# Kernel optimization log

Measured on AMD Instinct MI355X. Metric: run time of the kernel, lower is better.

The kernel has to match this reference:

```python
import jax, jax.numpy as jnp
import numpy as np

H = 16          # num_heads
D = 64          # head_dim = dim // num_heads
ROPE_THETA = 10000.0
NEG = -1e9


def _rope_angles(n, d):
    # matches get_1d_rotary_pos_embed(head_dim, N): freqs_cis = polar(1, t outer (theta^-(2i/d)))
    inv_freq = 1.0 / (ROPE_THETA ** (jnp.arange(0, d, 2, dtype=jnp.float32) / d))  # [d/2]
    ang = jnp.arange(n, dtype=jnp.float32)[:, None] * inv_freq[None, :]            # [n, d/2]
    return jnp.cos(ang), jnp.sin(ang)


def _apply_rope(x, cos, sin):
    # x: [B,H,N,D]; complex rotation on adjacent pairs (use_real=False semantics)
    x0 = x[..., 0::2]
    x1 = x[..., 1::2]
    # broadcast cos/sin [N, D/2] over batch and heads
    r0 = x0 * cos - x1 * sin
    r1 = x0 * sin + x1 * cos
    return jnp.stack([r0, r1], axis=-1).reshape(x.shape)


def setup_inputs() -> dict:
    key = jax.random.key(0)
    ks = jax.random.split(key, 5)
    B, N, C = 4, 2048, 1024
    s_in = 1.0 / np.sqrt(C)
    return {
        "x": jax.random.normal(ks[0], (B, N, C), dtype=jnp.float32),
        "Wqkv_w": jax.random.normal(ks[1], (3 * C, C), dtype=jnp.float32) * s_in,
        "Wqkv_b": jax.random.normal(ks[2], (3 * C,), dtype=jnp.float32) * 0.01,
        "out_w": jax.random.normal(ks[3], (C, C), dtype=jnp.float32) * s_in,
        "out_b": jax.random.normal(ks[4], (C,), dtype=jnp.float32) * 0.01,
    }


def reference(x, Wqkv_w, Wqkv_b, out_w, out_b):
    B, N, C = x.shape
    scale = D ** -0.5
    # fused QKV projection: [B,N,3C] -> [3,B,H,N,D]
    qkv = (jnp.einsum('bnc,oc->bno', x, Wqkv_w) + Wqkv_b)
    qkv = qkv.reshape(B, N, 3, H, D).transpose(2, 0, 3, 1, 4)
    q, k, v = qkv[0], qkv[1], qkv[2]
    # qk_norm=False -> Identity
    cos, sin = _rope_angles(N, D)
    q = _apply_rope(q, cos, sin)
    k = _apply_rope(k, cos, sin)
    attn = jnp.einsum('bhqd,bhkd->bhqk', q * scale, k)      # [B,H,N,N]
    causal = jnp.triu(jnp.ones((N, N), dtype=bool), k=1)
    attn = jnp.where(causal[None, None], NEG, attn)
    attn = jax.nn.softmax(attn, axis=-1)
    o = jnp.einsum('bhqk,bhkd->bhqd', attn, v)              # [B,H,N,D]
    o = o.transpose(0, 2, 1, 3).reshape(B, N, C)
    return jnp.einsum('bnc,oc->bno', o, out_w) + out_b
```

## Files before the change

kernel.cpp:

```cpp
#include <hip/hip_runtime.h>
#include <hip/hip_bf16.h>

#define DEVI __device__ __forceinline__

typedef __attribute__((ext_vector_type(8))) short short8v;
typedef __attribute__((ext_vector_type(4))) float f32x4;
typedef __attribute__((ext_vector_type(2))) unsigned u32x2;

DEVI short f2bf(float f) {
  __hip_bfloat16 h = __float2bfloat16(f);
  return __builtin_bit_cast(short, h);
}
DEVI float bf2f(short s) {
  unsigned u = ((unsigned)(unsigned short)s) << 16;
  return __builtin_bit_cast(float, u);
}
DEVI unsigned packbf(float a, float b) {
  return (unsigned)(unsigned short)f2bf(a) | ((unsigned)(unsigned short)f2bf(b) << 16);
}
DEVI void gload16(const void* g, void* l) {
  __builtin_amdgcn_global_load_lds((const __attribute__((address_space(1))) void*)g,
                                   (__attribute__((address_space(3))) void*)l, 16, 0, 0);
}
#define MFMA16(a, b, c) __builtin_amdgcn_mfma_f32_16x16x32_bf16((a), (b), (c), 0, 0, 0)


__global__ void cvt_all(const float* __restrict__ x, const float* __restrict__ wq,
                        const float* __restrict__ wo, short* __restrict__ xb,
                        short* __restrict__ wqb, short* __restrict__ wob) {
  int i = blockIdx.x * blockDim.x + threadIdx.x;
  const float* in;
  short* out;
  if (i < 2097152) { in = x; out = xb; }
  else if (i < 2097152 + 786432) { in = wq; out = wqb; i -= 2097152; }
  else { in = wo; out = wob; i -= 2097152 + 786432; }
  float4 v = ((const float4*)in)[i];
  short4 o;
  o.x = f2bf(v.x); o.y = f2bf(v.y); o.z = f2bf(v.z); o.w = f2bf(v.w);
  ((short4*)out)[i] = o;
}

__global__ void rope_table(float2* __restrict__ tbl) {
  int i = blockIdx.x * blockDim.x + threadIdx.x;
  int n = i >> 5, f = i & 31;
  float inv = powf(10000.0f, -(float)f * (1.0f / 32.0f));
  float ang = (float)n * inv;
  tbl[i] = make_float2(cosf(ang), sinf(ang));
}

__global__ void rope_k(short* __restrict__ kk, const float2* __restrict__ tbl) {
  int i = blockIdx.x * blockDim.x + threadIdx.x;
  int row = i >> 3, c8 = i & 7;
  int n = row & 2047;
  short* ad = kk + (size_t)row * 64 + c8 * 8;
  short8v vv = *(short8v*)ad;
  short8v ov;
#pragma unroll
  for (int j = 0; j < 4; ++j) {
    float2 cs = tbl[n * 32 + c8 * 4 + j];
    float x0 = bf2f(vv[2 * j]), x1 = bf2f(vv[2 * j + 1]);
    ov[2 * j]     = f2bf(x0 * cs.x - x1 * cs.y);
    ov[2 * j + 1] = f2bf(x0 * cs.y + x1 * cs.x);
  }
  *(short8v*)ad = ov;
}

__global__ __launch_bounds__(512, 2)
void gemm256(const short* __restrict__ A, const short* __restrict__ Bw,
             const float* __restrict__ bias,
             short* __restrict__ q, short* __restrict__ k, short* __restrict__ v,
             int Kdim) {
  __shared__ __attribute__((aligned(16))) short lds[32768];
  const int t = threadIdx.x;
  const int lane = t & 63, w = t >> 6;
  const int wr = w >> 2, wc = w & 3;
  const int g = lane >> 4, r16 = lane & 15;
  const int n0 = blockIdx.x * 256, m0 = blockIdx.y * 256;

  int goffs[2], loffs[2];
#pragma unroll
  for (int p = 0; p < 2; ++p) {
    int c = p * 512 + t;
    int row = c >> 2, u = c & 3;
    goffs[p] = row * Kdim + ((u ^ ((row >> 1) & 3)) * 8);
    loffs[p] = c * 16;
  }
  const short* Abase = A + (size_t)m0 * Kdim;
  const short* Bbase = Bw + (size_t)n0 * Kdim;

  auto STAGE = [&](int s, int k0) {
#pragma unroll
    for (int p = 0; p < 2; ++p) {
      gload16(Abase + k0 + goffs[p], (char*)lds + s * 32768 + loffs[p]);
      gload16(Bbase + k0 + goffs[p], (char*)lds + s * 32768 + 16384 + loffs[p]);
    }
  };

  f32x4 acc[8][4];
#pragma unroll
  for (int i = 0; i < 8; ++i)
#pragma unroll
    for (int j = 0; j < 4; ++j) acc[i][j] = (f32x4){0.f, 0.f, 0.f, 0.f};

  const int nsteps = Kdim >> 5;
  STAGE(0, 0);
  __syncthreads();

  const int rsw = (r16 >> 1) & 3;
  int cur = 0;
  for (int st = 0; st < nsteps; ++st) {
    if (st + 1 < nsteps) STAGE(cur ^ 1, (st + 1) << 5);
    const char* Ab = (const char*)lds + cur * 32768;
    const char* Bb = Ab + 16384;
    short8v bf[4];
#pragma unroll
    for (int ni = 0; ni < 4; ++ni) {
      int rowb = wc * 64 + ni * 16 + r16;
      bf[ni] = *(const short8v*)(Bb + rowb * 64 + ((g ^ rsw) << 4));
    }
#pragma unroll
    for (int mi = 0; mi < 8; ++mi) {
      int rowa = wr * 128 + mi * 16 + r16;
      short8v af = *(const short8v*)(Ab + rowa * 64 + ((g ^ rsw) << 4));
#pragma unroll
      for (int ni = 0; ni < 4; ++ni)
        acc[mi][ni] = MFMA16(af, bf[ni], acc[mi][ni]);
    }
    __syncthreads();
    cur ^= 1;
  }

  const int b = m0 >> 11, nb = m0 & 2047;
  if (n0 < 2048) {
#pragma unroll
    for (int ni = 0; ni < 4; ++ni) {
      int col = n0 + wc * 64 + ni * 16 + r16;
      float bv = bias[col];
      int s = col >> 10, h = (col & 1023) >> 6, d = col & 63;
      short* dst = (s == 0) ? q : k;
#pragma unroll
      for (int mi = 0; mi < 8; ++mi) {
        int mrow = m0 + wr * 128 + mi * 16 + g * 4;
#pragma unroll
        for (int r = 0; r < 4; ++r) {
          int n = (mrow + r) & 2047;
          dst[(((size_t)(b * 16 + h)) * 2048 + n) * 64 + d] = f2bf(acc[mi][ni][r] + bv);
        }
      }
    }
  } else {
    short* Cs = lds;
    const int hdrb = (n0 - 2048) >> 6;
#pragma unroll
    for (int hh = 0; hh < 4; ++hh) {
      if (wc == hh) {
#pragma unroll
        for (int ni = 0; ni < 4; ++ni) {
          float bv = bias[n0 + hh * 64 + ni * 16 + r16];
#pragma unroll
          for (int mi = 0; mi < 8; ++mi) {
            u32x2 pk;
            pk[0] = packbf(acc[mi][ni][0] + bv, acc[mi][ni][1] + bv);
            pk[1] = packbf(acc[mi][ni][2] + bv, acc[mi][ni][3] + bv);
            *(u32x2*)&Cs[(ni * 16 + r16) * 264 + wr * 128 + mi * 16 + g * 4] = pk;
          }
        }
      }
      __syncthreads();
      short* vdst = v + ((size_t)(b * 16 + hdrb + hh)) * 64 * 2048;
#pragma unroll
      for (int j = 0; j < 4; ++j) {
        int chunk = j * 512 + t;
        int d = chunk >> 5, c = chunk & 31;
        short8v val = *(const short8v*)&Cs[d * 264 + c * 8];
        *(short8v*)(vdst + (size_t)d * 2048 + nb + c * 8) = val;
      }
      __syncthreads();
    }
  }
}

__global__ __launch_bounds__(256)
void gemm_f32(const short* __restrict__ A, const short* __restrict__ Bw,
              const float* __restrict__ bias, float* __restrict__ fout,
              int Ndim, int Kdim) {
  __shared__ __attribute__((aligned(16))) short As[3][128 * 32];
  __shared__ __attribute__((aligned(16))) short Bs[3][128 * 32];
  const int t = threadIdx.x;
  const int lane = t & 63, w = t >> 6;
  const int wr = w >> 1, wc = w & 1;
  const int g = lane >> 4, r16 = lane & 15;
  const int m0 = blockIdx.y * 128, n0 = blockIdx.x * 128;

  int goffs[2], loffs[2];
#pragma unroll
  for (int p = 0; p < 2; ++p) {
    int c = p * 256 + t;
    int row = c >> 2, u = c & 3;
    goffs[p] = row * Kdim + ((u ^ ((row >> 1) & 3)) * 8);
    loffs[p] = c * 16;
  }
  const short* Abase = A + (size_t)m0 * Kdim;
  const short* Bbase = Bw + (size_t)n0 * Kdim;

  auto STAGE = [&](int s, int k0) {
#pragma unroll
    for (int p = 0; p < 2; ++p) {
      gload16(Abase + k0 + goffs[p], (char*)&As[s][0] + loffs[p]);
      gload16(Bbase + k0 + goffs[p], (char*)&Bs[s][0] + loffs[p]);
    }
  };

  f32x4 acc[4][4];
#pragma unroll
  for (int i = 0; i < 4; ++i)
#pragma unroll
    for (int j = 0; j < 4; ++j) acc[i][j] = (f32x4){0.f, 0.f, 0.f, 0.f};

  const int nsteps = Kdim >> 5;
  STAGE(0, 0);
  STAGE(1, 32);
  asm volatile("s_waitcnt vmcnt(4)" ::: "memory");
  __builtin_amdgcn_s_barrier();
  asm volatile("" ::: "memory");

  int cur = 0, pre = 2;
  const int rsw = (r16 >> 1) & 3;
  for (int st = 0; st < nsteps; ++st) {
    if (st + 2 < nsteps) STAGE(pre, (st + 2) << 5);
    short8v af[4], bf[4];
#pragma unroll
    for (int mi = 0; mi < 4; ++mi)
      af[mi] = *(const short8v*)&As[cur][(wr * 64 + mi * 16 + r16) * 32 +
                                         ((g ^ rsw) * 8)];
#pragma unroll
    for (int ni = 0; ni < 4; ++ni)
      bf[ni] = *(const short8v*)&Bs[cur][(wc * 64 + ni * 16 + r16) * 32 +
                                         ((g ^ rsw) * 8)];
#pragma unroll
    for (int mi = 0; mi < 4; ++mi)
#pragma unroll
      for (int ni = 0; ni < 4; ++ni)
        acc[mi][ni] = MFMA16(af[mi], bf[ni], acc[mi][ni]);
    if (st + 2 < nsteps) asm volatile("s_waitcnt vmcnt(4)" ::: "memory");
    else                 asm volatile("s_waitcnt vmcnt(0)" ::: "memory");
    __builtin_amdgcn_s_barrier();
    asm volatile("" ::: "memory");
    cur = (cur == 2) ? 0 : cur + 1;
    pre = (pre == 2) ? 0 : pre + 1;
  }

#pragma unroll
  for (int ni = 0; ni < 4; ++ni) {
    int col = n0 + wc * 64 + ni * 16 + r16;
    float bv = bias[col];
#pragma unroll
    for (int mi = 0; mi < 4; ++mi) {
      int mrow = m0 + wr * 64 + mi * 16 + g * 4;
#pragma unroll
      for (int r = 0; r < 4; ++r)
        fout[(size_t)(mrow + r) * Ndim + col] = acc[mi][ni][r] + bv;
    }
  }
}

__global__ __launch_bounds__(512)
void fattn(const short* __restrict__ q, const short* __restrict__ k,
           const short* __restrict__ vT, const float2* __restrict__ tbl,
           short* __restrict__ o) {
  const int bx = blockIdx.x;
  const int idx = bx >> 6;
  const int qt = (idx < 4) ? (7 - idx) : (idx - 4);
  const int bh = bx & 63;
  const int b = bh >> 4, h = bh & 15;
  const int t = threadIdx.x, lane = t & 63, w = t >> 6;
  const int g = lane >> 4, r16 = lane & 15;

  __shared__ __attribute__((aligned(16))) short Ks[2][64 * 64];
  __shared__ __attribute__((aligned(16))) short Vt[2][64 * 64];
  __shared__ __attribute__((aligned(16))) short Ps[8][2][16 * 72];

  const short* qb = q + (size_t)bh * 2048 * 64;
  const short* kb = k + (size_t)bh * 2048 * 64;
  const short* vb = vT + (size_t)bh * 2048 * 64;

  const int srow = t >> 3, su = t & 7;
  const int sx8 = (su ^ (srow & 7)) * 8;
  const int koff = srow * 64 + sx8;
  const int voff = srow * 2048 + sx8;
  const int loff = t * 16;
  auto STAGE = [&](int s, int kt) {
    gload16(kb + (size_t)kt * 4096 + koff, (char*)&Ks[s][0] + loff);
    gload16(vb + kt * 64 + voff, (char*)&Vt[s][0] + loff);
  };

  const int q0 = qt * 256 + w * 32;

  const float sc = 0.125f * 1.44269504088896f;
  short8v aq[2][2];
#pragma unroll
  for (int qi = 0; qi < 2; ++qi) {
    const int n = q0 + qi * 16 + r16;
#pragma unroll
    for (int dk = 0; dk < 2; ++dk) {
      short8v raw = *(const short8v*)(qb + (size_t)n * 64 + dk * 32 + g * 8);
      short8v rq;
#pragma unroll
      for (int j = 0; j < 4; ++j) {
        float2 cs = tbl[n * 32 + dk * 16 + g * 4 + j];
        float x0 = bf2f(raw[2 * j]), x1 = bf2f(raw[2 * j + 1]);
        rq[2 * j]     = f2bf((x0 * cs.x - x1 * cs.y) * sc);
        rq[2 * j + 1] = f2bf((x0 * cs.y + x1 * cs.x) * sc);
      }
      aq[qi][dk] = rq;
    }
  }

  const short one_bf = 0x3F80;
  const short8v ones = {one_bf, one_bf, one_bf, one_bf, one_bf, one_bf, one_bf, one_bf};
  const float M = 24.0f;

  f32x4 oacc[2][4], lacc[2];
#pragma unroll
  for (int qi = 0; qi < 2; ++qi) {
#pragma unroll
    for (int dc = 0; dc < 4; ++dc) oacc[qi][dc] = (f32x4){0.f, 0.f, 0.f, 0.f};
    lacc[qi] = (f32x4){0.f, 0.f, 0.f, 0.f};
  }

  const int ktmax = 4 * qt + 3;

  STAGE(0, 0);
  __syncthreads();

  for (int kt = 0; kt <= ktmax; ++kt) {
    const int cur = kt & 1;
    if (kt < ktmax) STAGE(cur ^ 1, kt + 1);

    const bool act0 = (kt * 64 <= q0 + 15);
    const bool act1 = (kt * 64 <= q0 + 31);

    f32x4 s[2][4];
#pragma unroll
    for (int qi = 0; qi < 2; ++qi)
#pragma unroll
      for (int kc = 0; kc < 4; ++kc) s[qi][kc] = (f32x4){0.f, 0.f, 0.f, 0.f};

    if (act1) {
      __builtin_amdgcn_s_setprio(1);
#pragma unroll
      for (int kc = 0; kc < 4; ++kc) {
        int key = kc * 16 + r16;
        const char* rb = (const char*)&Ks[cur][0] + key * 128;
        short8v kf0 = *(const short8v*)(rb + (((g) ^ (key & 7)) << 4));
        short8v kf1 = *(const short8v*)(rb + (((4 + g) ^ (key & 7)) << 4));
        if (act0) {
          s[0][kc] = MFMA16(kf0, aq[0][0], s[0][kc]);
          s[0][kc] = MFMA16(kf1, aq[0][1], s[0][kc]);
        }
        s[1][kc] = MFMA16(kf0, aq[1][0], s[1][kc]);
        s[1][kc] = MFMA16(kf1, aq[1][1], s[1][kc]);
      }
      __builtin_amdgcn_s_setprio(0);

#pragma unroll
      for (int qi = 0; qi < 2; ++qi) {
        if (qi == 0 && !act0) continue;
        const int qrow = q0 + qi * 16 + r16;
        const bool needmask = (kt * 64 + 63 > q0 + qi * 16);
        if (needmask) {
#pragma unroll
          for (int kc = 0; kc < 4; ++kc)
#pragma unroll
            for (int r = 0; r < 4; ++r)
              if (kt * 64 + kc * 16 + g * 4 + r > qrow) s[qi][kc][r] = -1e30f;
        }
        unsigned pk[4][2];
#pragma unroll
        for (int kc = 0; kc < 4; ++kc) {
          float p0 = __builtin_amdgcn_exp2f(s[qi][kc][0] - M);
          float p1 = __builtin_amdgcn_exp2f(s[qi][kc][1] - M);
          float p2 = __builtin_amdgcn_exp2f(s[qi][kc][2] - M);
          float p3 = __builtin_amdgcn_exp2f(s[qi][kc][3] - M);
          pk[kc][0] = packbf(p0, p1);
          pk[kc][1] = packbf(p2, p3);
        }
#pragma unroll
        for (int kc = 0; kc < 4; ++kc)
          *(u32x2*)((char*)&Ps[w][qi][0] + r16 * 144 + kc * 32 + g * 8) =
              (u32x2){pk[kc][0], pk[kc][1]};
      }

      asm volatile("" ::: "memory");

      short8v pa[2][2];
#pragma unroll
      for (int qi = 0; qi < 2; ++qi) {
        if (qi == 0 && !act0) continue;
#pragma unroll
        for (int kk = 0; kk < 2; ++kk)
          pa[qi][kk] =
              *(const short8v*)((char*)&Ps[w][qi][0] + r16 * 144 + kk * 64 + g * 16);
      }
      __builtin_amdgcn_s_setprio(1);
      if (act0) {
        lacc[0] = MFMA16(pa[0][0], ones, lacc[0]);
        lacc[0] = MFMA16(pa[0][1], ones, lacc[0]);
      }
      lacc[1] = MFMA16(pa[1][0], ones, lacc[1]);
      lacc[1] = MFMA16(pa[1][1], ones, lacc[1]);
#pragma unroll
      for (int dc = 0; dc < 4; ++dc) {
        int d = dc * 16 + r16;
        const char* vr = (const char*)&Vt[cur][0] + d * 128;
#pragma unroll
        for (int kk = 0; kk < 2; ++kk) {
          short8v bv = *(const short8v*)(vr + (((kk * 4 + g) ^ (d & 7)) << 4));
          if (act0) oacc[0][dc] = MFMA16(pa[0][kk], bv, oacc[0][dc]);
          oacc[1][dc] = MFMA16(pa[1][kk], bv, oacc[1][dc]);
        }
      }
      __builtin_amdgcn_s_setprio(0);
    }
    __syncthreads();
  }

#pragma unroll
  for (int qi = 0; qi < 2; ++qi) {
#pragma unroll
    for (int r = 0; r < 4; ++r) {
      float ilr = 1.f / lacc[qi][r];
      int qg = q0 + qi * 16 + g * 4 + r;
      short* orow = o + ((size_t)(b * 2048 + qg)) * 1024 + h * 64;
#pragma unroll
      for (int dc = 0; dc < 4; ++dc)
        orow[dc * 16 + r16] = f2bf(oacc[qi][dc][r] * ilr);
    }
  }
}

extern "C" void kernel_launch(void* const* d_in, const int* in_sizes, int n_in,
                              void* d_out, int out_size, void* d_ws, size_t ws_size,
                              hipStream_t stream) {
  const float* x    = (const float*)d_in[0];
  const float* Wqkv = (const float*)d_in[1];
  const float* bqkv = (const float*)d_in[2];
  const float* Wout = (const float*)d_in[3];
  const float* bout = (const float*)d_in[4];

  char* p = (char*)d_ws;
  short* xb = (short*)p;    p += (size_t)8192 * 1024 * 2;
  short* wqkvb = (short*)p; p += (size_t)3072 * 1024 * 2;
  short* woutb = (short*)p; p += (size_t)1024 * 1024 * 2;
  short* qbf = (short*)p;   p += (size_t)64 * 2048 * 64 * 2;
  short* kbf = (short*)p;   p += (size_t)64 * 2048 * 64 * 2;
  short* vbf = (short*)p;   p += (size_t)64 * 2048 * 64 * 2;
  float2* tbl = (float2*)p; p += (size_t)2048 * 32 * 8;

  cvt_all<<<12288, 256, 0, stream>>>(x, Wqkv, Wout, xb, wqkvb, woutb);
  rope_table<<<256, 256, 0, stream>>>(tbl);

  gemm256<<<dim3(12, 32), 512, 0, stream>>>(xb, wqkvb, bqkv, qbf, kbf, vbf, 1024);
  rope_k<<<4096, 256, 0, stream>>>(kbf, tbl);
  fattn<<<dim3(512), 512, 0, stream>>>(qbf, kbf, vbf, tbl, xb);
  gemm_f32<<<dim3(8, 64), 256, 0, stream>>>(xb, woutb, bout, (float*)d_out, 1024, 1024);
}
```

Baseline: 188.2 us.

## Switch attention to 32x32 MFMA with permlane P reshuffle; widen GEMM K-step

The attention kernel now uses 32x32x16 bf16 MFMAs. Its S fragments are converted into the A operand for the PV product in registers via v_permlane32_swap, which removes the per-wave LDS round trip for P. The QKV GEMM doubles its K step per stage to 64, doubles LDS use to 128KB, and uses a new XOR swizzle, so it needs fewer barriers per K. The larger LDS footprint may reduce occupancy of the launch_bounds(512,2) GEMM, and the coarser 32-row causal granularity drops the act0 skip.

Measured after the change: 183.6 us. -2.4%, faster.

```diff
diff --git a/kernel.cpp b/kernel.cpp
--- a/kernel.cpp
+++ b/kernel.cpp
@@ -5,7 +5,9 @@
 
 typedef __attribute__((ext_vector_type(8))) short short8v;
 typedef __attribute__((ext_vector_type(4))) float f32x4;
+typedef __attribute__((ext_vector_type(16))) float f32x16;
 typedef __attribute__((ext_vector_type(2))) unsigned u32x2;
+typedef __attribute__((ext_vector_type(4))) unsigned u32x4;
 
 DEVI short f2bf(float f) {
   __hip_bfloat16 h = __float2bfloat16(f);
@@ -23,6 +25,8 @@
                                    (__attribute__((address_space(3))) void*)l, 16, 0, 0);
 }
 #define MFMA16(a, b, c) __builtin_amdgcn_mfma_f32_16x16x32_bf16((a), (b), (c), 0, 0, 0)
+#define MFMA32(a, b, c) __builtin_amdgcn_mfma_f32_32x32x16_bf16((a), (b), (c), 0, 0, 0)
+#define PLSWAP(a, b) asm("v_permlane32_swap_b32 %0, %1" : "+v"(a), "+v"(b))
 
 
 __global__ void cvt_all(const float* __restrict__ x, const float* __restrict__ wq,
@@ -70,19 +74,19 @@
              const float* __restrict__ bias,
              short* __restrict__ q, short* __restrict__ k, short* __restrict__ v,
              int Kdim) {
-  __shared__ __attribute__((aligned(16))) short lds[32768];
+  __shared__ __attribute__((aligned(16))) short lds[65536];
   const int t = threadIdx.x;
   const int lane = t & 63, w = t >> 6;
   const int wr = w >> 2, wc = w & 3;
   const int g = lane >> 4, r16 = lane & 15;
   const int n0 = blockIdx.x * 256, m0 = blockIdx.y * 256;
 
-  int goffs[2], loffs[2];
-#pragma unroll
-  for (int p = 0; p < 2; ++p) {
+  int goffs[4], loffs[4];
+#pragma unroll
+  for (int p = 0; p < 4; ++p) {
     int c = p * 512 + t;
-    int row = c >> 2, u = c & 3;
-    goffs[p] = row * Kdim + ((u ^ ((row >> 1) & 3)) * 8);
+    int row = c >> 3, u = c & 7;
+    goffs[p] = row * Kdim + ((u ^ (row & 7)) * 8);
     loffs[p] = c * 16;
   }
   const short* Abase = A + (size_t)m0 * Kdim;
@@ -90,9 +94,9 @@
 
   auto STAGE = [&](int s, int k0) {
 #pragma unroll
-    for (int p = 0; p < 2; ++p) {
+    for (int p = 0; p < 4; ++p) {
       gload16(Abase + k0 + goffs[p], (char*)lds + s * 32768 + loffs[p]);
-      gload16(Bbase + k0 + goffs[p], (char*)lds + s * 32768 + 16384 + loffs[p]);
+      gload16(Bbase + k0 + goffs[p], (char*)lds + 65536 + s * 32768 + loffs[p]);
     }
   };
 
@@ -102,29 +106,32 @@
 #pragma unroll
     for (int j = 0; j < 4; ++j) acc[i][j] = (f32x4){0.f, 0.f, 0.f, 0.f};
 
-  const int nsteps = Kdim >> 5;
+  const int nsteps = Kdim >> 6;
   STAGE(0, 0);
   __syncthreads();
 
-  const int rsw = (r16 >> 1) & 3;
   int cur = 0;
   for (int st = 0; st < nsteps; ++st) {
-    if (st + 1 < nsteps) STAGE(cur ^ 1, (st + 1) << 5);
+    if (st + 1 < nsteps) STAGE(cur ^ 1, (st + 1) << 6);
     const char* Ab = (const char*)lds + cur * 32768;
-    const char* Bb = Ab + 16384;
-    short8v bf[4];
-#pragma unroll
-    for (int ni = 0; ni < 4; ++ni) {
-      int rowb = wc * 64 + ni * 16 + r16;
-      bf[ni] = *(const short8v*)(Bb + rowb * 64 + ((g ^ rsw) << 4));
-    }
-#pragma unroll
-    for (int mi = 0; mi < 8; ++mi) {
-      int rowa = wr * 128 + mi * 16 + r16;
-      short8v af = *(const short8v*)(Ab + rowa * 64 + ((g ^ rsw) << 4));
-#pragma unroll
-      for (int ni = 0; ni < 4; ++ni)
-        acc[mi][ni] = MFMA16(af, bf[ni], acc[mi][ni]);
+    const char* Bb = (const char*)lds + 65536 + cur * 32768;
+#pragma unroll
+    for (int ks = 0; ks < 2; ++ks) {
+      short8v bf[4];
+#pragma unroll
+      for (int ni = 0; ni < 4; ++ni) {
+        int rowb = wc * 64 + ni * 16 + r16;
+        bf[ni] = *(const short8v*)(Bb + rowb * 128 + (((ks * 4 + g) ^ (rowb & 7)) << 4));
+      }
+#pragma unroll
+      for (int mi = 0; mi < 8; ++mi) {
+        int rowa = wr * 128 + mi * 16 + r16;
+        short8v af =
+            *(const short8v*)(Ab + rowa * 128 + (((ks * 4 + g) ^ (rowa & 7)) << 4));
+#pragma unroll
+        for (int ni = 0; ni < 4; ++ni)
+          acc[mi][ni] = MFMA16(af, bf[ni], acc[mi][ni]);
+      }
     }
     __syncthreads();
     cur ^= 1;
@@ -274,11 +281,11 @@
   const int bh = bx & 63;
   const int b = bh >> 4, h = bh & 15;
   const int t = threadIdx.x, lane = t & 63, w = t >> 6;
-  const int g = lane >> 4, r16 = lane & 15;
+  const int q32 = lane & 31, hi = lane >> 5;
+  const int hi4 = hi * 4;
 
   __shared__ __attribute__((aligned(16))) short Ks[2][64 * 64];
   __shared__ __attribute__((aligned(16))) short Vt[2][64 * 64];
-  __shared__ __attribute__((aligned(16))) short Ps[8][2][16 * 72];
 
   const short* qb = q + (size_t)bh * 2048 * 64;
   const short* kb = k + (size_t)bh * 2048 * 64;
@@ -294,39 +301,32 @@
     gload16(vb + kt * 64 + voff, (char*)&Vt[s][0] + loff);
   };
 
-  const int q0 = qt * 256 + w * 32;
+  const int q0w = qt * 256 + w * 32;
+  const int nrow = q0w + q32;
 
   const float sc = 0.125f * 1.44269504088896f;
-  short8v aq[2][2];
-#pragma unroll
-  for (int qi = 0; qi < 2; ++qi) {
-    const int n = q0 + qi * 16 + r16;
-#pragma unroll
-    for (int dk = 0; dk < 2; ++dk) {
-      short8v raw = *(const short8v*)(qb + (size_t)n * 64 + dk * 32 + g * 8);
-      short8v rq;
-#pragma unroll
-      for (int j = 0; j < 4; ++j) {
-        float2 cs = tbl[n * 32 + dk * 16 + g * 4 + j];
-        float x0 = bf2f(raw[2 * j]), x1 = bf2f(raw[2 * j + 1]);
-        rq[2 * j]     = f2bf((x0 * cs.x - x1 * cs.y) * sc);
-        rq[2 * j + 1] = f2bf((x0 * cs.y + x1 * cs.x) * sc);
-      }
-      aq[qi][dk] = rq;
-    }
+  short8v aq[4];
+#pragma unroll
+  for (int ds = 0; ds < 4; ++ds) {
+    short8v raw = *(const short8v*)(qb + (size_t)nrow * 64 + ds * 16 + hi * 8);
+    short8v rq;
+#pragma unroll
+    for (int j = 0; j < 4; ++j) {
+      float2 cs = tbl[nrow * 32 + ds * 8 + hi4 + j];
+      float x0 = bf2f(raw[2 * j]), x1 = bf2f(raw[2 * j + 1]);
+      rq[2 * j]     = f2bf((x0 * cs.x - x1 * cs.y) * sc);
+      rq[2 * j + 1] = f2bf((x0 * cs.y + x1 * cs.x) * sc);
+    }
+    aq[ds] = rq;
   }
 
   const short one_bf = 0x3F80;
   const short8v ones = {one_bf, one_bf, one_bf, one_bf, one_bf, one_bf, one_bf, one_bf};
   const float M = 24.0f;
 
-  f32x4 oacc[2][4], lacc[2];
-#pragma unroll
-  for (int qi = 0; qi < 2; ++qi) {
-#pragma unroll
-    for (int dc = 0; dc < 4; ++dc) oacc[qi][dc] = (f32x4){0.f, 0.f, 0.f, 0.f};
-    lacc[qi] = (f32x4){0.f, 0.f, 0.f, 0.f};
-  }
+  f32x16 oacc[2], lacc;
+#pragma unroll
+  for (int j = 0; j < 16; ++j) { oacc[0][j] = 0.f; oacc[1][j] = 0.f; lacc[j] = 0.f; }
 
   const int ktmax = 4 * qt + 3;
 
@@ -337,87 +337,73 @@
     const int cur = kt & 1;
     if (kt < ktmax) STAGE(cur ^ 1, kt + 1);
 
-    const bool act0 = (kt * 64 <= q0 + 15);
-    const bool act1 = (kt * 64 <= q0 + 31);
-
-    f32x4 s[2][4];
-#pragma unroll
-    for (int qi = 0; qi < 2; ++qi)
-#pragma unroll
-      for (int kc = 0; kc < 4; ++kc) s[qi][kc] = (f32x4){0.f, 0.f, 0.f, 0.f};
-
-    if (act1) {
+    if (kt * 64 <= q0w + 31) {
+      f32x16 s[2];
+#pragma unroll
+      for (int j = 0; j < 16; ++j) { s[0][j] = 0.f; s[1][j] = 0.f; }
       __builtin_amdgcn_s_setprio(1);
 #pragma unroll
-      for (int kc = 0; kc < 4; ++kc) {
-        int key = kc * 16 + r16;
-        const char* rb = (const char*)&Ks[cur][0] + key * 128;
-        short8v kf0 = *(const short8v*)(rb + (((g) ^ (key & 7)) << 4));
-        short8v kf1 = *(const short8v*)(rb + (((4 + g) ^ (key & 7)) << 4));
-        if (act0) {
-          s[0][kc] = MFMA16(kf0, aq[0][0], s[0][kc]);
-          s[0][kc] = MFMA16(kf1, aq[0][1], s[0][kc]);
-        }
-        s[1][kc] = MFMA16(kf0, aq[1][0], s[1][kc]);
-        s[1][kc] = MFMA16(kf1, aq[1][1], s[1][kc]);
+      for (int ds = 0; ds < 4; ++ds) {
+        int u = 2 * ds + hi;
+#pragma unroll
+        for (int kbl = 0; kbl < 2; ++kbl) {
+          int key = kbl * 32 + q32;
+          short8v kf = *(const short8v*)((const char*)&Ks[cur][0] + key * 128 +
+                                         ((u ^ (key & 7)) << 4));
+          s[kbl] = MFMA32(kf, aq[ds], s[kbl]);
+        }
       }
       __builtin_amdgcn_s_setprio(0);
 
-#pragma unroll
-      for (int qi = 0; qi < 2; ++qi) {
-        if (qi == 0 && !act0) continue;
-        const int qrow = q0 + qi * 16 + r16;
-        const bool needmask = (kt * 64 + 63 > q0 + qi * 16);
+      const bool needmask = (kt * 64 + 63 > q0w);
+      unsigned pa[4][4];
+#pragma unroll
+      for (int kbl = 0; kbl < 2; ++kbl) {
         if (needmask) {
 #pragma unroll
-          for (int kc = 0; kc < 4; ++kc)
-#pragma unroll
-            for (int r = 0; r < 4; ++r)
-              if (kt * 64 + kc * 16 + g * 4 + r > qrow) s[qi][kc][r] = -1e30f;
-        }
-        unsigned pk[4][2];
-#pragma unroll
-        for (int kc = 0; kc < 4; ++kc) {
-          float p0 = __builtin_amdgcn_exp2f(s[qi][kc][0] - M);
-          float p1 = __builtin_amdgcn_exp2f(s[qi][kc][1] - M);
-          float p2 = __builtin_amdgcn_exp2f(s[qi][kc][2] - M);
-          float p3 = __builtin_amdgcn_exp2f(s[qi][kc][3] - M);
-          pk[kc][0] = packbf(p0, p1);
-          pk[kc][1] = packbf(p2, p3);
-        }
-#pragma unroll
-        for (int kc = 0; kc < 4; ++kc)
-          *(u32x2*)((char*)&Ps[w][qi][0] + r16 * 144 + kc * 32 + g * 8) =
-              (u32x2){pk[kc][0], pk[kc][1]};
-      }
-
-      asm volatile("" ::: "memory");
-
-      short8v pa[2][2];
-#pragma unroll
-      for (int qi = 0; qi < 2; ++qi) {
-        if (qi == 0 && !act0) continue;
-#pragma unroll
-        for (int kk = 0; kk < 2; ++kk)
-          pa[qi][kk] =
-              *(const short8v*)((char*)&Ps[w][qi][0] + r16 * 144 + kk * 64 + g * 16);
-      }
+          for (int r = 0; r < 16; ++r) {
+            int keyg = kt * 64 + kbl * 32 + (r & 3) + 8 * (r >> 2) + hi4;
+            if (keyg > nrow) s[kbl][r] = -1e30f;
+          }
+        }
+        unsigned pk[8];
+#pragma unroll
+        for (int p = 0; p < 8; ++p) {
+          float p0 = __builtin_amdgcn_exp2f(s[kbl][2 * p] - M);
+          float p1 = __builtin_amdgcn_exp2f(s[kbl][2 * p + 1] - M);
+          pk[p] = packbf(p0, p1);
+        }
+        {
+          unsigned x0 = pk[0], x1 = pk[2];
+          unsigned y0 = pk[1], y1 = pk[3];
+          PLSWAP(x0, x1);
+          PLSWAP(y0, y1);
+          pa[kbl * 2][0] = x0; pa[kbl * 2][1] = y0;
+          pa[kbl * 2][2] = x1; pa[kbl * 2][3] = y1;
+        }
+        {
+          unsigned x0 = pk[4], x1 = pk[6];
+          unsigned y0 = pk[5], y1 = pk[7];
+          PLSWAP(x0, x1);
+          PLSWAP(y0, y1);
+          pa[kbl * 2 + 1][0] = x0; pa[kbl * 2 + 1][1] = y0;
+          pa[kbl * 2 + 1][2] = x1; pa[kbl * 2 + 1][3] = y1;
+        }
+      }
+
       __builtin_amdgcn_s_setprio(1);
-      if (act0) {
-        lacc[0] = MFMA16(pa[0][0], ones, lacc[0]);
-        lacc[0] = MFMA16(pa[0][1], ones, lacc[0]);
-      }
-      lacc[1] = MFMA16(pa[1][0], ones, lacc[1]);
-      lacc[1] = MFMA16(pa[1][1], ones, lacc[1]);
-#pragma unroll
-      for (int dc = 0; dc < 4; ++dc) {
-        int d = dc * 16 + r16;
-        const char* vr = (const char*)&Vt[cur][0] + d * 128;
-#pragma unroll
-        for (int kk = 0; kk < 2; ++kk) {
-          short8v bv = *(const short8v*)(vr + (((kk * 4 + g) ^ (d & 7)) << 4));
-          if (act0) oacc[0][dc] = MFMA16(pa[0][kk], bv, oacc[0][dc]);
-          oacc[1][dc] = MFMA16(pa[1][kk], bv, oacc[1][dc]);
+#pragma unroll
+      for (int kk = 0; kk < 4; ++kk) {
+        short8v paf = __builtin_bit_cast(
+            short8v, (u32x4){pa[kk][0], pa[kk][1], pa[kk][2], pa[kk][3]});
+        lacc = MFMA32(paf, ones, lacc);
+        int u = 2 * kk + hi;
+#pragma unroll
+        for (int db = 0; db < 2; ++db) {
+          int d = db * 32 + q32;
+          short8v vf = *(const short8v*)((const char*)&Vt[cur][0] + d * 128 +
+                                         ((u ^ (d & 7)) << 4));
+          oacc[db] = MFMA32(paf, vf, oacc[db]);
         }
       }
       __builtin_amdgcn_s_setprio(0);
@@ -426,16 +412,12 @@
   }
 
 #pragma unroll
-  for (int qi = 0; qi < 2; ++qi) {
-#pragma unroll
-    for (int r = 0; r < 4; ++r) {
-      float ilr = 1.f / lacc[qi][r];
-      int qg = q0 + qi * 16 + g * 4 + r;
-      short* orow = o + ((size_t)(b * 2048 + qg)) * 1024 + h * 64;
-#pragma unroll
-      for (int dc = 0; dc < 4; ++dc)
-        orow[dc * 16 + r16] = f2bf(oacc[qi][dc][r] * ilr);
-    }
+  for (int r = 0; r < 16; ++r) {
+    float ilr = 1.f / lacc[r];
+    int qg = q0w + (r & 3) + 8 * (r >> 2) + hi4;
+    short* orow = o + ((size_t)(b * 2048 + qg)) * 1024 + h * 64;
+    orow[q32]      = f2bf(oacc[0][r] * ilr);
+    orow[32 + q32] = f2bf(oacc[1][r] * ilr);
   }
 }
 
```
